# Kernel tuning notes

Measured on AMD Instinct MI355X. Metric: run time of the kernel, lower is better.

Reference implementation:

```python
import jax, jax.numpy as jnp
import numpy as np

N, E, G = 50000, 400000, 64
IN_CH, HID, H, EDGE_DIM = 128, 64, 4, 4
NEG_SLOPE = 0.2


def setup_inputs() -> dict:
    key = jax.random.key(0)
    ks = list(jax.random.split(key, 40))
    kit = iter(ks)

    def rn(shape, scale=0.05):
        return jax.random.normal(next(kit), shape, dtype=jnp.float32) * scale

    inp = {
        "x": jax.random.normal(next(kit), (N, IN_CH), dtype=jnp.float32),
        "edge_attr": jax.random.uniform(next(kit), (E, 2), dtype=jnp.float32),
        "edge_index": jax.random.randint(next(kit), (2, E), 0, N),
        "batch": jnp.sort(jax.random.randint(next(kit), (N,), 0, G)),
    }
    # edge feature fusion MLPs
    inp["W_et"] = rn((1, EDGE_DIM // 2)); inp["b_et"] = jnp.zeros((EDGE_DIM // 2,), jnp.float32)
    inp["W_uw"] = rn((1, EDGE_DIM // 2)); inp["b_uw"] = jnp.zeros((EDGE_DIM // 2,), jnp.float32)
    inp["W_ua"] = rn((1, 1));             inp["b_ua"] = jnp.zeros((1,), jnp.float32)
    # two GATv2 layers
    for li, ic in ((0, IN_CH), (1, HID)):
        inp[f"Wl{li}"] = rn((ic, H * HID)); inp[f"bl{li}"] = jnp.zeros((H * HID,), jnp.float32)
        inp[f"Wr{li}"] = rn((ic, H * HID)); inp[f"br{li}"] = jnp.zeros((H * HID,), jnp.float32)
        inp[f"att{li}"] = rn((H, HID))
        inp[f"We{li}"] = rn((EDGE_DIM, H * HID))
        inp[f"bias{li}"] = jnp.zeros((HID,), jnp.float32)
    # heads
    inp["W_fc"] = rn((HID, HID)); inp["b_fc"] = jnp.zeros((HID,), jnp.float32)
    inp["W_res"] = rn((HID, 1)); inp["b_res"] = jnp.zeros((1,), jnp.float32)
    inp["W_time"] = rn((HID, 1)); inp["b_time"] = jnp.zeros((1,), jnp.float32)
    return inp


def gatv2_layer(x, src, dst, edge_attr_proj, Wl, bl, Wr, br, att, We, bias):
    # GATv2Conv, concat=False (mean over heads)
    xl = (x @ Wl + bl).reshape(-1, H, HID)   # [N,H,C] transformed source feats
    xr = (x @ Wr + br).reshape(-1, H, HID)   # [N,H,C] transformed target feats
    ee = (edge_attr_proj @ We).reshape(-1, H, HID)  # [E,H,C]
    xj = xl[src]                              # per-edge gather of source
    m = jax.nn.leaky_relu(xj + xr[dst] + ee, NEG_SLOPE)  # [E,H,C]
    score = jnp.einsum('ehc,hc->eh', m, att)  # [E,H]
    # segment softmax over incoming edges of each destination node
    smax = jax.ops.segment_max(score, dst, num_segments=N)  # [N,H]
    ex = jnp.exp(score - smax[dst])
    denom = jax.ops.segment_sum(ex, dst, num_segments=N)
    alpha = ex / (denom[dst] + 1e-16)         # [E,H]
    out = jax.ops.segment_sum(xj * alpha[..., None], dst, num_segments=N)  # [N,H,C]
    return out.mean(axis=1) + bias            # [N,C]


def reference(x, edge_attr, W_et, b_et, W_uw, b_uw, W_ua, b_ua,
              Wl0, bl0, Wr0, br0, att0, We0, bias0,
              Wl1, bl1, Wr1, br1, att1, We1, bias1,
              W_fc, b_fc, W_res, b_res, W_time, b_time,
              edge_index, batch):
    src, dst = edge_index[0], edge_index[1]
    edge_type = edge_attr[:, 0:1]
    unwind = edge_attr[:, 1:2]
    et_emb = edge_type @ W_et + b_et
    uw_emb = unwind @ W_uw + b_uw
    uw_att = jax.nn.sigmoid(unwind @ W_ua + b_ua)
    eap = jnp.concatenate([et_emb, uw_emb * uw_att], axis=-1)  # [E,4]

    h = jax.nn.relu(gatv2_layer(x, src, dst, eap, Wl0, bl0, Wr0, br0, att0, We0, bias0))
    h = jax.nn.relu(gatv2_layer(h, src, dst, eap, Wl1, bl1, Wr1, br1, att1, We1, bias1))

    # global mean pool over graphs (dropout is identity at inference)
    sums = jax.ops.segment_sum(h, batch, num_segments=G)
    cnts = jax.ops.segment_sum(jnp.ones((h.shape[0],), h.dtype), batch, num_segments=G)
    pooled = sums / jnp.maximum(cnts, 1.0)[:, None]
    g = jax.nn.relu(pooled @ W_fc + b_fc)
    result = g @ W_res + b_res
    time = g @ W_time + b_time
    return jnp.concatenate([result, time], axis=1)  # [G,2]
```

## Files before the change

kernel.cpp:

```cpp
#include <hip/hip_runtime.h>
#include <math.h>

namespace {

constexpr int N = 50000;
constexpr int E = 400000;
constexpr int G = 64;
constexpr int HID = 64;
constexpr int HH = 256;
constexpr int NCT = 32;
constexpr float NEG = 0.2f;
constexpr int GAT_BLOCKS = 2048;
constexpr int GAT_WAVES = GAT_BLOCKS * 4;

typedef __attribute__((ext_vector_type(8))) short short8v;
typedef __attribute__((ext_vector_type(4))) float f32x4;

__device__ __forceinline__ unsigned short f2bf(float f) {
    unsigned int u = __float_as_uint(f);
    u += 0x7FFFu + ((u >> 16) & 1u);
    return (unsigned short)(u >> 16);
}
__device__ __forceinline__ float bf2f(unsigned short h) {
    return __uint_as_float(((unsigned int)h) << 16);
}
__device__ __forceinline__ float4 ld_bf4(const unsigned short* p) {
    uint2 u = *(const uint2*)p;
    float4 r;
    r.x = __uint_as_float(u.x << 16);
    r.y = __uint_as_float(u.x & 0xFFFF0000u);
    r.z = __uint_as_float(u.y << 16);
    r.w = __uint_as_float(u.y & 0xFFFF0000u);
    return r;
}

__global__ __launch_bounds__(256) void hist_k(
    const int* __restrict__ dst, int* __restrict__ deg, int* __restrict__ rank)
{
    int e = blockIdx.x * 256 + threadIdx.x;
    if (e < E) rank[e] = atomicAdd(&deg[dst[e]], 1);
}

__global__ __launch_bounds__(256) void scan1_k(
    const int* __restrict__ deg, int* __restrict__ pre, int* __restrict__ bsum)
{
    __shared__ int s[256];
    int i = blockIdx.x * 256 + threadIdx.x;
    int v = (i < N) ? deg[i] : 0;
    s[threadIdx.x] = v;
    __syncthreads();
    for (int off = 1; off < 256; off <<= 1) {
        int t = (threadIdx.x >= off) ? s[threadIdx.x - off] : 0;
        __syncthreads();
        s[threadIdx.x] += t;
        __syncthreads();
    }
    if (i < N) pre[i] = s[threadIdx.x] - v;
    if (threadIdx.x == 255) bsum[blockIdx.x] = s[255];
}

__global__ __launch_bounds__(256) void scan2_k(int* __restrict__ bsum, int nb)
{
    __shared__ int s[256];
    int tid = threadIdx.x;
    int v = (tid < nb) ? bsum[tid] : 0;
    s[tid] = v;
    __syncthreads();
    for (int off = 1; off < 256; off <<= 1) {
        int t = (tid >= off) ? s[tid - off] : 0;
        __syncthreads();
        s[tid] += t;
        __syncthreads();
    }
    if (tid < nb) bsum[tid] = s[tid] - v;
}

__global__ __launch_bounds__(256) void scatter_k(
    const int* __restrict__ src, const int* __restrict__ dst,
    const float* __restrict__ ea,
    const float* __restrict__ W_et, const float* __restrict__ b_et,
    const float* __restrict__ W_uw, const float* __restrict__ b_uw,
    const float* __restrict__ W_ua, const float* __restrict__ b_ua,
    const int* __restrict__ pre, const int* __restrict__ bsum,
    const int* __restrict__ rank,
    int* __restrict__ csr_src, float* __restrict__ eap_csr)
{
    int e = blockIdx.x * 256 + threadIdx.x;
    if (e >= E) return;
    float et = ea[e * 2 + 0], uw = ea[e * 2 + 1];
    float ua = 1.f / (1.f + expf(-(uw * W_ua[0] + b_ua[0])));
    float4 v;
    v.x = et * W_et[0] + b_et[0];
    v.y = et * W_et[1] + b_et[1];
    v.z = (uw * W_uw[0] + b_uw[0]) * ua;
    v.w = (uw * W_uw[1] + b_uw[1]) * ua;
    int d = dst[e];
    int pos = pre[d] + bsum[d >> 8] + rank[e];
    csr_src[pos] = src[e];
    *(float4*)&eap_csr[(size_t)pos * 4] = v;
}

__global__ __launch_bounds__(256) void pack_k(
    const float* __restrict__ Wl0, const float* __restrict__ Wr0,
    const float* __restrict__ bl0, const float* __restrict__ br0,
    const float* __restrict__ Wl1, const float* __restrict__ Wr1,
    const float* __restrict__ bl1, const float* __restrict__ br1,
    unsigned short* __restrict__ w0hi, unsigned short* __restrict__ w0lo,
    unsigned short* __restrict__ w1hi, unsigned short* __restrict__ w1lo,
    float* __restrict__ bc0, float* __restrict__ bc1)
{
    int idx = blockIdx.x * 256 + threadIdx.x;
    if (idx < 8192) {
        int lane = idx & 63, ct = (idx >> 6) & 31, kt = idx >> 11;
        int col = ct * 16 + (lane & 15);
        const float* W = (col < 256) ? Wl0 : Wr0;
        int c = col & 255;
        int kb = kt * 32 + ((lane >> 4) & 3) * 8;
#pragma unroll
        for (int e = 0; e < 8; e++) {
            float v = W[(size_t)(kb + e) * 256 + c];
            unsigned short hi = f2bf(v);
            unsigned short lo = f2bf(v - bf2f(hi));
            w0hi[(size_t)idx * 8 + e] = hi;
            w0lo[(size_t)idx * 8 + e] = lo;
        }
    } else if (idx < 8192 + 4096) {
        int s = idx - 8192;
        int lane = s & 63, ct = (s >> 6) & 31, kt = s >> 11;
        int col = ct * 16 + (lane & 15);
        const float* W = (col < 256) ? Wl1 : Wr1;
        int c = col & 255;
        int kb = kt * 32 + ((lane >> 4) & 3) * 8;
#pragma unroll
        for (int e = 0; e < 8; e++) {
            float v = W[(size_t)(kb + e) * 256 + c];
            unsigned short hi = f2bf(v);
            unsigned short lo = f2bf(v - bf2f(hi));
            w1hi[(size_t)s * 8 + e] = hi;
            w1lo[(size_t)s * 8 + e] = lo;
        }
    } else if (idx < 8192 + 4096 + 512) {
        int i = idx - (8192 + 4096);
        bc0[i] = (i < 256) ? bl0[i] : br0[i - 256];
    } else if (idx < 8192 + 4096 + 1024) {
        int i = idx - (8192 + 4096 + 512);
        bc1[i] = (i < 256) ? bl1[i] : br1[i - 256];
    }
}

template <int IC>
__global__ __launch_bounds__(256) void projmm_k(
    const float* __restrict__ x,
    const unsigned short* __restrict__ whi, const unsigned short* __restrict__ wlo,
    const float* __restrict__ bc,
    unsigned short* __restrict__ xlb, unsigned short* __restrict__ xrb)
{
    constexpr int KT = IC / 32;
    constexpr int LDX = IC + 4;
    constexpr int SROW = 516;
    constexpr int XS_BYTES = 32 * LDX * 4;
    constexpr int ST_BYTES = 16 * SROW * 2;
    constexpr int SMEM_BYTES = (XS_BYTES > ST_BYTES) ? XS_BYTES : ST_BYTES;
    __shared__ char smem[SMEM_BYTES];
    float (*xs)[LDX] = (float (*)[LDX])smem;
    const int base = blockIdx.x * 32;
    const int tid = threadIdx.x;
    for (int idx = tid; idx < 32 * IC / 4; idx += 256) {
        int j = idx / (IC / 4), k4 = idx - j * (IC / 4);
        int n = base + j;
        float4 v = make_float4(0.f, 0.f, 0.f, 0.f);
        if (n < N) v = *(const float4*)&x[(size_t)n * IC + k4 * 4];
        *(float4*)&xs[j][k4 * 4] = v;
    }
    __syncthreads();
    const int w = tid >> 6, lane = tid & 63;
    const int lr = lane & 15, lg = lane >> 4;
    f32x4 acc[2][8];
#pragma unroll
    for (int rt = 0; rt < 2; rt++)
#pragma unroll
        for (int ct = 0; ct < 8; ct++) {
            f32x4 z = {0.f, 0.f, 0.f, 0.f};
            acc[rt][ct] = z;
        }
#pragma unroll
    for (int kt = 0; kt < KT; kt++) {
        short8v ahi[2], alo[2];
#pragma unroll
        for (int rt = 0; rt < 2; rt++) {
            const float* p = &xs[rt * 16 + lr][kt * 32 + lg * 8];
            float4 v0 = *(const float4*)p;
            float4 v1 = *(const float4*)(p + 4);
            float fv[8] = {v0.x, v0.y, v0.z, v0.w, v1.x, v1.y, v1.z, v1.w};
            short8v h, l;
#pragma unroll
            for (int e = 0; e < 8; e++) {
                unsigned short hb = f2bf(fv[e]);
                h[e] = (short)hb;
                l[e] = (short)f2bf(fv[e] - bf2f(hb));
            }
            ahi[rt] = h;
            alo[rt] = l;
        }
        const size_t bbase = ((size_t)(kt * NCT + w * 8) * 64 + lane) * 8;
#pragma unroll
        for (int ct = 0; ct < 8; ct++) {
            short8v bhi = *(const short8v*)&whi[bbase + (size_t)ct * 64 * 8];
            short8v blo = *(const short8v*)&wlo[bbase + (size_t)ct * 64 * 8];
#pragma unroll
            for (int rt = 0; rt < 2; rt++) {
                acc[rt][ct] = __builtin_amdgcn_mfma_f32_16x16x32_bf16(ahi[rt], bhi, acc[rt][ct], 0, 0, 0);
                acc[rt][ct] = __builtin_amdgcn_mfma_f32_16x16x32_bf16(alo[rt], bhi, acc[rt][ct], 0, 0, 0);
                acc[rt][ct] = __builtin_amdgcn_mfma_f32_16x16x32_bf16(ahi[rt], blo, acc[rt][ct], 0, 0, 0);
            }
        }
    }
    __syncthreads();
    unsigned short* st = (unsigned short*)smem;
#pragma unroll
    for (int rt = 0; rt < 2; rt++) {
#pragma unroll
        for (int ct = 0; ct < 8; ct++) {
            int col = (w * 8 + ct) * 16 + lr;
            float bv = bc[col];
            f32x4 a = acc[rt][ct];
#pragma unroll
            for (int i = 0; i < 4; i++) {
                st[(lg * 4 + i) * SROW + col] = f2bf(a[i] + bv);
            }
        }
        __syncthreads();
        int rbase = base + rt * 16;
#pragma unroll
        for (int k = 0; k < 4; k++) {
            int ci = tid + k * 256;
            int rl = ci >> 6;
            int cc = (ci & 63) * 8;
            int rg = rbase + rl;
            if (rg < N) {
                uint2 lo = *(const uint2*)&st[rl * SROW + cc];
                uint2 hi = *(const uint2*)&st[rl * SROW + cc + 4];
                uint4 val = make_uint4(lo.x, lo.y, hi.x, hi.y);
                if (cc < 256) *(uint4*)&xlb[(size_t)rg * HH + cc] = val;
                else          *(uint4*)&xrb[(size_t)rg * HH + (cc - 256)] = val;
            }
        }
        __syncthreads();
    }
}

__global__ __launch_bounds__(256) void gat_aggr_k(
    const unsigned short* __restrict__ xlb, const unsigned short* __restrict__ xrb,
    const float* __restrict__ eap_csr, const float* __restrict__ We,
    const float* __restrict__ att,
    const int* __restrict__ pre, const int* __restrict__ bsum,
    const int* __restrict__ deg,
    const int* __restrict__ csr_src,
    const float* __restrict__ bias, float* __restrict__ hout)
{
    const int lane = threadIdx.x & 63;
    const int c4 = lane * 4;
    const float4 w0 = *(const float4*)&We[0 * HH + c4];
    const float4 w1 = *(const float4*)&We[1 * HH + c4];
    const float4 w2 = *(const float4*)&We[2 * HH + c4];
    const float4 w3 = *(const float4*)&We[3 * HH + c4];
    const float4 av = *(const float4*)&att[c4];
    float4 bb = make_float4(0.f, 0.f, 0.f, 0.f);
    if (lane < 16) bb = *(const float4*)&bias[c4];

    const int wid = __builtin_amdgcn_readfirstlane(blockIdx.x * 4 + (threadIdx.x >> 6));
    constexpr int q = N / GAT_WAVES;
    constexpr int r = N % GAT_WAVES;
    int d0 = wid * q + (wid < r ? wid : r);
    int dcnt = q + (wid < r ? 1 : 0);

    for (int d = d0; d < d0 + dcnt; ++d) {
        int start = pre[d] + bsum[d >> 8];
        int end = start + deg[d];
        const float4 vr = ld_bf4(&xrb[(size_t)d * HH + c4]);
        float denom = 0.f;
        float ax = 0.f, ay = 0.f, az = 0.f, aw = 0.f;
        int idx = start;
        for (; idx + 4 <= end; idx += 4) {
            int s0 = csr_src[idx], s1 = csr_src[idx + 1];
            int s2 = csr_src[idx + 2], s3 = csr_src[idx + 3];
            float4 a0 = *(const float4*)&eap_csr[(size_t)(idx + 0) * 4];
            float4 a1 = *(const float4*)&eap_csr[(size_t)(idx + 1) * 4];
            float4 a2 = *(const float4*)&eap_csr[(size_t)(idx + 2) * 4];
            float4 a3 = *(const float4*)&eap_csr[(size_t)(idx + 3) * 4];
            float4 vl0 = ld_bf4(&xlb[(size_t)s0 * HH + c4]);
            float4 vl1 = ld_bf4(&xlb[(size_t)s1 * HH + c4]);
            float4 vl2 = ld_bf4(&xlb[(size_t)s2 * HH + c4]);
            float4 vl3 = ld_bf4(&xlb[(size_t)s3 * HH + c4]);
            float p0, p1, p2, p3;
            {
                float q0 = vl0.x + vr.x + a0.x * w0.x + a0.y * w1.x + a0.z * w2.x + a0.w * w3.x;
                float q1 = vl0.y + vr.y + a0.x * w0.y + a0.y * w1.y + a0.z * w2.y + a0.w * w3.y;
                float q2 = vl0.z + vr.z + a0.x * w0.z + a0.y * w1.z + a0.z * w2.z + a0.w * w3.z;
                float q3 = vl0.w + vr.w + a0.x * w0.w + a0.y * w1.w + a0.z * w2.w + a0.w * w3.w;
                q0 = fmaxf(q0, NEG * q0); q1 = fmaxf(q1, NEG * q1);
                q2 = fmaxf(q2, NEG * q2); q3 = fmaxf(q3, NEG * q3);
                p0 = q0 * av.x + q1 * av.y + q2 * av.z + q3 * av.w;
            }
            {
                float q0 = vl1.x + vr.x + a1.x * w0.x + a1.y * w1.x + a1.z * w2.x + a1.w * w3.x;
                float q1 = vl1.y + vr.y + a1.x * w0.y + a1.y * w1.y + a1.z * w2.y + a1.w * w3.y;
                float q2 = vl1.z + vr.z + a1.x * w0.z + a1.y * w1.z + a1.z * w2.z + a1.w * w3.z;
                float q3 = vl1.w + vr.w + a1.x * w0.w + a1.y * w1.w + a1.z * w2.w + a1.w * w3.w;
                q0 = fmaxf(q0, NEG * q0); q1 = fmaxf(q1, NEG * q1);
                q2 = fmaxf(q2, NEG * q2); q3 = fmaxf(q3, NEG * q3);
                p1 = q0 * av.x + q1 * av.y + q2 * av.z + q3 * av.w;
            }
            {
                float q0 = vl2.x + vr.x + a2.x * w0.x + a2.y * w1.x + a2.z * w2.x + a2.w * w3.x;
                float q1 = vl2.y + vr.y + a2.x * w0.y + a2.y * w1.y + a2.z * w2.y + a2.w * w3.y;
                float q2 = vl2.z + vr.z + a2.x * w0.z + a2.y * w1.z + a2.z * w2.z + a2.w * w3.z;
                float q3 = vl2.w + vr.w + a2.x * w0.w + a2.y * w1.w + a2.z * w2.w + a2.w * w3.w;
                q0 = fmaxf(q0, NEG * q0); q1 = fmaxf(q1, NEG * q1);
                q2 = fmaxf(q2, NEG * q2); q3 = fmaxf(q3, NEG * q3);
                p2 = q0 * av.x + q1 * av.y + q2 * av.z + q3 * av.w;
            }
            {
                float q0 = vl3.x + vr.x + a3.x * w0.x + a3.y * w1.x + a3.z * w2.x + a3.w * w3.x;
                float q1 = vl3.y + vr.y + a3.x * w0.y + a3.y * w1.y + a3.z * w2.y + a3.w * w3.y;
                float q2 = vl3.z + vr.z + a3.x * w0.z + a3.y * w1.z + a3.z * w2.z + a3.w * w3.z;
                float q3 = vl3.w + vr.w + a3.x * w0.w + a3.y * w1.w + a3.z * w2.w + a3.w * w3.w;
                q0 = fmaxf(q0, NEG * q0); q1 = fmaxf(q1, NEG * q1);
                q2 = fmaxf(q2, NEG * q2); q3 = fmaxf(q3, NEG * q3);
                p3 = q0 * av.x + q1 * av.y + q2 * av.z + q3 * av.w;
            }
#pragma unroll
            for (int off = 1; off <= 8; off <<= 1) {
                p0 += __shfl_xor(p0, off, 64);
                p1 += __shfl_xor(p1, off, 64);
                p2 += __shfl_xor(p2, off, 64);
                p3 += __shfl_xor(p3, off, 64);
            }
            float e0 = __expf(p0);
            float e1 = __expf(p1);
            float e2 = __expf(p2);
            float e3 = __expf(p3);
            denom += e0 + e1 + e2 + e3;
            ax += e0 * vl0.x + e1 * vl1.x + e2 * vl2.x + e3 * vl3.x;
            ay += e0 * vl0.y + e1 * vl1.y + e2 * vl2.y + e3 * vl3.y;
            az += e0 * vl0.z + e1 * vl1.z + e2 * vl2.z + e3 * vl3.z;
            aw += e0 * vl0.w + e1 * vl1.w + e2 * vl2.w + e3 * vl3.w;
        }
        for (; idx < end; ++idx) {
            int s = csr_src[idx];
            float4 a = *(const float4*)&eap_csr[(size_t)idx * 4];
            float4 vl = ld_bf4(&xlb[(size_t)s * HH + c4]);
            float q0 = vl.x + vr.x + a.x * w0.x + a.y * w1.x + a.z * w2.x + a.w * w3.x;
            float q1 = vl.y + vr.y + a.x * w0.y + a.y * w1.y + a.z * w2.y + a.w * w3.y;
            float q2 = vl.z + vr.z + a.x * w0.z + a.y * w1.z + a.z * w2.z + a.w * w3.z;
            float q3 = vl.w + vr.w + a.x * w0.w + a.y * w1.w + a.z * w2.w + a.w * w3.w;
            q0 = fmaxf(q0, NEG * q0); q1 = fmaxf(q1, NEG * q1);
            q2 = fmaxf(q2, NEG * q2); q3 = fmaxf(q3, NEG * q3);
            float p = q0 * av.x + q1 * av.y + q2 * av.z + q3 * av.w;
#pragma unroll
            for (int off = 1; off <= 8; off <<= 1) p += __shfl_xor(p, off, 64);
            float e = __expf(p);
            denom += e;
            ax += e * vl.x;
            ay += e * vl.y;
            az += e * vl.z;
            aw += e * vl.w;
        }
        float inv = 0.25f / (denom + 1e-16f);
        ax *= inv; ay *= inv; az *= inv; aw *= inv;
        ax += __shfl_xor(ax, 16, 64); ax += __shfl_xor(ax, 32, 64);
        ay += __shfl_xor(ay, 16, 64); ay += __shfl_xor(ay, 32, 64);
        az += __shfl_xor(az, 16, 64); az += __shfl_xor(az, 32, 64);
        aw += __shfl_xor(aw, 16, 64); aw += __shfl_xor(aw, 32, 64);
        if (lane < 16) {
            float4 o;
            o.x = fmaxf(ax + bb.x, 0.f);
            o.y = fmaxf(ay + bb.y, 0.f);
            o.z = fmaxf(az + bb.z, 0.f);
            o.w = fmaxf(aw + bb.w, 0.f);
            *(float4*)&hout[(size_t)d * HID + c4] = o;
        }
    }
}

__global__ __launch_bounds__(256) void pool_k(
    const float* __restrict__ h, const int* __restrict__ batch,
    float* __restrict__ pooled)
{
    constexpr int CH = 16;
    int c = threadIdx.x & 63;
    int chunk = blockIdx.x * 4 + (threadIdx.x >> 6);
    int n0 = chunk * CH;
    if (n0 >= N) return;
    int nend = (n0 + CH < N) ? n0 + CH : N;
    float sum = 0.f;
    int curb = batch[n0];
    for (int n = n0; n < nend; ++n) {
        int b = batch[n];
        if (b != curb) {
            atomicAdd(&pooled[curb * HID + c], sum);
            sum = 0.f; curb = b;
        }
        sum += h[(size_t)n * HID + c];
    }
    atomicAdd(&pooled[curb * HID + c], sum);
}

__global__ __launch_bounds__(64) void head_k(
    const float* __restrict__ pooled, const int* __restrict__ batch,
    const float* __restrict__ W_fc, const float* __restrict__ b_fc,
    const float* __restrict__ W_res, const float* __restrict__ b_res,
    const float* __restrict__ W_time, const float* __restrict__ b_time,
    float* __restrict__ out)
{
    int g = blockIdx.x;
    int c = threadIdx.x;
    int lo = 0, hi = N;
    while (lo < hi) { int mid = (lo + hi) >> 1; if (batch[mid] < g) lo = mid + 1; else hi = mid; }
    int start = lo;
    hi = N;
    while (lo < hi) { int mid = (lo + hi) >> 1; if (batch[mid] < g + 1) lo = mid + 1; else hi = mid; }
    int end = lo;
    float cnt = (float)(end - start);
    float p = pooled[g * HID + c] / fmaxf(cnt, 1.0f);
    __shared__ float ps[HID];
    ps[c] = p;
    __syncthreads();
    float gv = b_fc[c];
    for (int k = 0; k < HID; k++) gv += ps[k] * W_fc[k * HID + c];
    gv = fmaxf(gv, 0.f);
    float r = gv * W_res[c];
    float t = gv * W_time[c];
#pragma unroll
    for (int off = 32; off > 0; off >>= 1) {
        r += __shfl_down(r, off, 64);
        t += __shfl_down(t, off, 64);
    }
    if (c == 0) {
        out[g * 2 + 0] = r + b_res[0];
        out[g * 2 + 1] = t + b_time[0];
    }
}

}

extern "C" void kernel_launch(void* const* d_in, const int* in_sizes, int n_in,
                              void* d_out, int out_size, void* d_ws, size_t ws_size,
                              hipStream_t stream) {
    const float* x         = (const float*)d_in[0];
    const float* edge_attr = (const float*)d_in[1];
    const int*   edge_index= (const int*)d_in[2];
    const int*   batch     = (const int*)d_in[3];
    const float* W_et = (const float*)d_in[4];
    const float* b_et = (const float*)d_in[5];
    const float* W_uw = (const float*)d_in[6];
    const float* b_uw = (const float*)d_in[7];
    const float* W_ua = (const float*)d_in[8];
    const float* b_ua = (const float*)d_in[9];
    const float* Wl0  = (const float*)d_in[10];
    const float* bl0  = (const float*)d_in[11];
    const float* Wr0  = (const float*)d_in[12];
    const float* br0  = (const float*)d_in[13];
    const float* att0 = (const float*)d_in[14];
    const float* We0  = (const float*)d_in[15];
    const float* bias0= (const float*)d_in[16];
    const float* Wl1  = (const float*)d_in[17];
    const float* bl1  = (const float*)d_in[18];
    const float* Wr1  = (const float*)d_in[19];
    const float* br1  = (const float*)d_in[20];
    const float* att1 = (const float*)d_in[21];
    const float* We1  = (const float*)d_in[22];
    const float* bias1= (const float*)d_in[23];
    const float* W_fc = (const float*)d_in[24];
    const float* b_fc = (const float*)d_in[25];
    const float* W_res= (const float*)d_in[26];
    const float* b_res= (const float*)d_in[27];
    const float* W_time=(const float*)d_in[28];
    const float* b_time=(const float*)d_in[29];

    const int* src = edge_index;
    const int* dst = edge_index + E;

    float* ws    = (float*)d_ws;
    unsigned short* xlb = (unsigned short*)ws;
    unsigned short* xrb = (unsigned short*)(ws + (size_t)N * HH);
    float* h1    = ws  + (size_t)2 * N * HH;
    float* h2    = h1  + (size_t)N * HID;
    float* pooled= h2  + (size_t)N * HID;
    int*   deg      = (int*)(pooled + (size_t)G * HID);
    int*   pre      = deg + N;
    int*   bsum     = pre + N;
    int*   rank     = bsum + 256;
    int*   csr_src  = rank + E;
    float* eap_csr  = (float*)(csr_src + E);
    unsigned short* w0hi = (unsigned short*)rank;
    unsigned short* w0lo = w0hi + 65536;
    unsigned short* w1hi = w0lo + 65536;
    unsigned short* w1lo = w1hi + 32768;
    float* bc0 = (float*)(w1lo + 32768);
    float* bc1 = bc0 + 512;

    dim3 b256(256);
    const int NB = (N + 255) / 256;
    const int NPROJ = (N + 31) / 32;

    hipMemsetAsync(pooled, 0, (size_t)(G * HID + N) * 4, stream);
    hist_k<<<(E + 255) / 256, b256, 0, stream>>>(dst, deg, rank);
    scan1_k<<<NB, b256, 0, stream>>>(deg, pre, bsum);
    scan2_k<<<1, b256, 0, stream>>>(bsum, NB);
    scatter_k<<<(E + 255) / 256, b256, 0, stream>>>(
        src, dst, edge_attr, W_et, b_et, W_uw, b_uw, W_ua, b_ua,
        pre, bsum, rank, csr_src, eap_csr);
    pack_k<<<52, b256, 0, stream>>>(Wl0, Wr0, bl0, br0, Wl1, Wr1, bl1, br1,
                                    w0hi, w0lo, w1hi, w1lo, bc0, bc1);

    projmm_k<128><<<NPROJ, b256, 0, stream>>>(x, w0hi, w0lo, bc0, xlb, xrb);
    gat_aggr_k<<<GAT_BLOCKS, b256, 0, stream>>>(
        xlb, xrb, eap_csr, We0, att0, pre, bsum, deg, csr_src, bias0, h1);

    projmm_k<64><<<NPROJ, b256, 0, stream>>>(h1, w1hi, w1lo, bc1, xlb, xrb);
    gat_aggr_k<<<GAT_BLOCKS, b256, 0, stream>>>(
        xlb, xrb, eap_csr, We1, att1, pre, bsum, deg, csr_src, bias1, h2);

    pool_k<<<((N + 15) / 16 + 3) / 4, b256, 0, stream>>>(h2, batch, pooled);
    head_k<<<G, dim3(64), 0, stream>>>(
        pooled, batch, W_fc, b_fc, W_res, b_res, W_time, b_time, (float*)d_out);
}
```

Before: 366.5 us.

## Fuse CSR construction into first-layer projection kernels to overlap and cut launches

The edge-degree histogram now runs as extra blocks of the first half of the layer-0 projection. The prefix scan runs as a single extra block of the second half. The memset is folded into the weight-pack kernel, and the two-level scan is replaced by one block that scans per-thread chunks, which removes the bsum indirection. The aim is to hide the small CSR-building kernels behind the projection GEMM and to remove several launches and serialization points. The costs are a fully serial per-thread chunk scan in one block and moving the packed weights into the unused half of the xr buffer.

```diff
diff --git a/kernel.cpp b/kernel.cpp
--- a/kernel.cpp
+++ b/kernel.cpp
@@ -13,6 +13,15 @@
 constexpr int GAT_BLOCKS = 2048;
 constexpr int GAT_WAVES = GAT_BLOCKS * 4;
 
+constexpr int NPROJ = (N + 31) / 32;
+constexpr int PH1 = 782;
+constexpr int PH1_ROWS = PH1 * 32;
+constexpr int PH2 = NPROJ - PH1;
+constexpr int HIST_BLOCKS = (E + 255) / 256;
+constexpr int PACK_BLOCKS = 52;
+constexpr int ZERO_ELEMS = G * HID + N;
+constexpr int ZERO_BLOCKS = (ZERO_ELEMS + 255) / 256;
+
 typedef __attribute__((ext_vector_type(8))) short short8v;
 typedef __attribute__((ext_vector_type(4))) float f32x4;
 
@@ -34,82 +43,23 @@
     return r;
 }
 
-__global__ __launch_bounds__(256) void hist_k(
-    const int* __restrict__ dst, int* __restrict__ deg, int* __restrict__ rank)
-{
-    int e = blockIdx.x * 256 + threadIdx.x;
-    if (e < E) rank[e] = atomicAdd(&deg[dst[e]], 1);
-}
-
-__global__ __launch_bounds__(256) void scan1_k(
-    const int* __restrict__ deg, int* __restrict__ pre, int* __restrict__ bsum)
-{
-    __shared__ int s[256];
-    int i = blockIdx.x * 256 + threadIdx.x;
-    int v = (i < N) ? deg[i] : 0;
-    s[threadIdx.x] = v;
-    __syncthreads();
-    for (int off = 1; off < 256; off <<= 1) {
-        int t = (threadIdx.x >= off) ? s[threadIdx.x - off] : 0;
-        __syncthreads();
-        s[threadIdx.x] += t;
-        __syncthreads();
-    }
-    if (i < N) pre[i] = s[threadIdx.x] - v;
-    if (threadIdx.x == 255) bsum[blockIdx.x] = s[255];
-}
-
-__global__ __launch_bounds__(256) void scan2_k(int* __restrict__ bsum, int nb)
-{
-    __shared__ int s[256];
-    int tid = threadIdx.x;
-    int v = (tid < nb) ? bsum[tid] : 0;
-    s[tid] = v;
-    __syncthreads();
-    for (int off = 1; off < 256; off <<= 1) {
-        int t = (tid >= off) ? s[tid - off] : 0;
-        __syncthreads();
-        s[tid] += t;
-        __syncthreads();
-    }
-    if (tid < nb) bsum[tid] = s[tid] - v;
-}
-
-__global__ __launch_bounds__(256) void scatter_k(
-    const int* __restrict__ src, const int* __restrict__ dst,
-    const float* __restrict__ ea,
-    const float* __restrict__ W_et, const float* __restrict__ b_et,
-    const float* __restrict__ W_uw, const float* __restrict__ b_uw,
-    const float* __restrict__ W_ua, const float* __restrict__ b_ua,
-    const int* __restrict__ pre, const int* __restrict__ bsum,
-    const int* __restrict__ rank,
-    int* __restrict__ csr_src, float* __restrict__ eap_csr)
-{
-    int e = blockIdx.x * 256 + threadIdx.x;
-    if (e >= E) return;
-    float et = ea[e * 2 + 0], uw = ea[e * 2 + 1];
-    float ua = 1.f / (1.f + expf(-(uw * W_ua[0] + b_ua[0])));
-    float4 v;
-    v.x = et * W_et[0] + b_et[0];
-    v.y = et * W_et[1] + b_et[1];
-    v.z = (uw * W_uw[0] + b_uw[0]) * ua;
-    v.w = (uw * W_uw[1] + b_uw[1]) * ua;
-    int d = dst[e];
-    int pos = pre[d] + bsum[d >> 8] + rank[e];
-    csr_src[pos] = src[e];
-    *(float4*)&eap_csr[(size_t)pos * 4] = v;
-}
-
-__global__ __launch_bounds__(256) void pack_k(
+__global__ __launch_bounds__(256) void prep_k(
     const float* __restrict__ Wl0, const float* __restrict__ Wr0,
     const float* __restrict__ bl0, const float* __restrict__ br0,
     const float* __restrict__ Wl1, const float* __restrict__ Wr1,
     const float* __restrict__ bl1, const float* __restrict__ br1,
     unsigned short* __restrict__ w0hi, unsigned short* __restrict__ w0lo,
     unsigned short* __restrict__ w1hi, unsigned short* __restrict__ w1lo,
-    float* __restrict__ bc0, float* __restrict__ bc1)
-{
-    int idx = blockIdx.x * 256 + threadIdx.x;
+    float* __restrict__ bc0, float* __restrict__ bc1,
+    int* __restrict__ zero_base)
+{
+    int b = blockIdx.x;
+    if (b >= PACK_BLOCKS) {
+        int i = (b - PACK_BLOCKS) * 256 + threadIdx.x;
+        if (i < ZERO_ELEMS) zero_base[i] = 0;
+        return;
+    }
+    int idx = b * 256 + threadIdx.x;
     if (idx < 8192) {
         int lane = idx & 63, ct = (idx >> 6) & 31, kt = idx >> 11;
         int col = ct * 16 + (lane & 15);
@@ -149,7 +99,8 @@
 }
 
 template <int IC>
-__global__ __launch_bounds__(256) void projmm_k(
+__device__ __forceinline__ void proj_body(
+    int base,
     const float* __restrict__ x,
     const unsigned short* __restrict__ whi, const unsigned short* __restrict__ wlo,
     const float* __restrict__ bc,
@@ -163,7 +114,6 @@
     constexpr int SMEM_BYTES = (XS_BYTES > ST_BYTES) ? XS_BYTES : ST_BYTES;
     __shared__ char smem[SMEM_BYTES];
     float (*xs)[LDX] = (float (*)[LDX])smem;
-    const int base = blockIdx.x * 32;
     const int tid = threadIdx.x;
     for (int idx = tid; idx < 32 * IC / 4; idx += 256) {
         int j = idx / (IC / 4), k4 = idx - j * (IC / 4);
@@ -249,12 +199,93 @@
     }
 }
 
+__global__ __launch_bounds__(256) void k1_projhist_k(
+    const float* __restrict__ x,
+    const unsigned short* __restrict__ whi, const unsigned short* __restrict__ wlo,
+    const float* __restrict__ bc,
+    unsigned short* __restrict__ xlb, unsigned short* __restrict__ xrb,
+    const int* __restrict__ dst, int* __restrict__ deg, int* __restrict__ rank)
+{
+    if (blockIdx.x < PH1) {
+        proj_body<128>(blockIdx.x * 32, x, whi, wlo, bc, xlb, xrb);
+    } else {
+        int e = (blockIdx.x - PH1) * 256 + threadIdx.x;
+        if (e < E) rank[e] = atomicAdd(&deg[dst[e]], 1);
+    }
+}
+
+__global__ __launch_bounds__(256) void k2_projscan_k(
+    const float* __restrict__ x,
+    const unsigned short* __restrict__ whi, const unsigned short* __restrict__ wlo,
+    const float* __restrict__ bc,
+    unsigned short* __restrict__ xlb, unsigned short* __restrict__ xrb,
+    const int* __restrict__ deg, int* __restrict__ pre)
+{
+    if (blockIdx.x < PH2) {
+        proj_body<128>(PH1_ROWS + blockIdx.x * 32, x, whi, wlo, bc, xlb, xrb);
+    } else {
+        constexpr int CH = 196;
+        __shared__ int sums[256];
+        int t = threadIdx.x;
+        int cbase = t * CH;
+        int cend = (cbase + CH < N) ? cbase + CH : N;
+        int s = 0;
+        for (int i = cbase; i < cend; ++i) s += deg[i];
+        sums[t] = s;
+        __syncthreads();
+        for (int off = 1; off < 256; off <<= 1) {
+            int tv = (t >= off) ? sums[t - off] : 0;
+            __syncthreads();
+            sums[t] += tv;
+            __syncthreads();
+        }
+        int run = sums[t] - s;
+        for (int i = cbase; i < cend; ++i) {
+            pre[i] = run;
+            run += deg[i];
+        }
+    }
+}
+
+__global__ __launch_bounds__(256) void scatter_k(
+    const int* __restrict__ src, const int* __restrict__ dst,
+    const float* __restrict__ ea,
+    const float* __restrict__ W_et, const float* __restrict__ b_et,
+    const float* __restrict__ W_uw, const float* __restrict__ b_uw,
+    const float* __restrict__ W_ua, const float* __restrict__ b_ua,
+    const int* __restrict__ pre, const int* __restrict__ rank,
+    int* __restrict__ csr_src, float* __restrict__ eap_csr)
+{
+    int e = blockIdx.x * 256 + threadIdx.x;
+    if (e >= E) return;
+    float et = ea[e * 2 + 0], uw = ea[e * 2 + 1];
+    float ua = 1.f / (1.f + expf(-(uw * W_ua[0] + b_ua[0])));
+    float4 v;
+    v.x = et * W_et[0] + b_et[0];
+    v.y = et * W_et[1] + b_et[1];
+    v.z = (uw * W_uw[0] + b_uw[0]) * ua;
+    v.w = (uw * W_uw[1] + b_uw[1]) * ua;
+    int d = dst[e];
+    int pos = pre[d] + rank[e];
+    csr_src[pos] = src[e];
+    *(float4*)&eap_csr[(size_t)pos * 4] = v;
+}
+
+template <int IC>
+__global__ __launch_bounds__(256) void projmm_k(
+    const float* __restrict__ x,
+    const unsigned short* __restrict__ whi, const unsigned short* __restrict__ wlo,
+    const float* __restrict__ bc,
+    unsigned short* __restrict__ xlb, unsigned short* __restrict__ xrb)
+{
+    proj_body<IC>(blockIdx.x * 32, x, whi, wlo, bc, xlb, xrb);
+}
+
 __global__ __launch_bounds__(256) void gat_aggr_k(
     const unsigned short* __restrict__ xlb, const unsigned short* __restrict__ xrb,
     const float* __restrict__ eap_csr, const float* __restrict__ We,
     const float* __restrict__ att,
-    const int* __restrict__ pre, const int* __restrict__ bsum,
-    const int* __restrict__ deg,
+    const int* __restrict__ pre, const int* __restrict__ deg,
     const int* __restrict__ csr_src,
     const float* __restrict__ bias, float* __restrict__ hout)
 {
@@ -275,7 +306,7 @@
     int dcnt = q + (wid < r ? 1 : 0);
 
     for (int d = d0; d < d0 + dcnt; ++d) {
-        int start = pre[d] + bsum[d >> 8];
+        int start = pre[d];
         int end = start + deg[d];
         const float4 vr = ld_bf4(&xrb[(size_t)d * HH + c4]);
         float denom = 0.f;
@@ -482,8 +513,15 @@
     const int* dst = edge_index + E;
 
     float* ws    = (float*)d_ws;
-    unsigned short* xlb = (unsigned short*)ws;
-    unsigned short* xrb = (unsigned short*)(ws + (size_t)N * HH);
+    unsigned short* xlb  = (unsigned short*)ws;
+    float* xr_reg = ws + (size_t)N * HH;
+    unsigned short* xrb  = (unsigned short*)xr_reg;
+    unsigned short* w0hi = (unsigned short*)xr_reg + (size_t)N * HH;
+    unsigned short* w0lo = w0hi + 65536;
+    unsigned short* w1hi = w0lo + 65536;
+    unsigned short* w1lo = w1hi + 32768;
+    float* bc0 = (float*)(w1lo + 32768);
+    float* bc1 = bc0 + 512;
     float* h1    = ws  + (size_t)2 * N * HH;
     float* h2    = h1  + (size_t)N * HID;
     float* pooled= h2  + (size_t)N * HID;
@@ -493,34 +531,29 @@
     int*   rank     = bsum + 256;
     int*   csr_src  = rank + E;
     float* eap_csr  = (float*)(csr_src + E);
-    unsigned short* w0hi = (unsigned short*)rank;
-    unsigned short* w0lo = w0hi + 65536;
-    unsigned short* w1hi = w0lo + 65536;
-    unsigned short* w1lo = w1hi + 32768;
-    float* bc0 = (float*)(w1lo + 32768);
-    float* bc1 = bc0 + 512;
 
     dim3 b256(256);
-    const int NB = (N + 255) / 256;
-    const int NPROJ = (N + 31) / 32;
-
-    hipMemsetAsync(pooled, 0, (size_t)(G * HID + N) * 4, stream);
-    hist_k<<<(E + 255) / 256, b256, 0, stream>>>(dst, deg, rank);
-    scan1_k<<<NB, b256, 0, stream>>>(deg, pre, bsum);
-    scan2_k<<<1, b256, 0, stream>>>(bsum, NB);
-    scatter_k<<<(E + 255) / 256, b256, 0, stream>>>(
+
+    prep_k<<<PACK_BLOCKS + ZERO_BLOCKS, b256, 0, stream>>>(
+        Wl0, Wr0, bl0, br0, Wl1, Wr1, bl1, br1,
+        w0hi, w0lo, w1hi, w1lo, bc0, bc1, (int*)pooled);
+
+    k1_projhist_k<<<PH1 + HIST_BLOCKS, b256, 0, stream>>>(
+        x, w0hi, w0lo, bc0, xlb, xrb, dst, deg, rank);
+
+    k2_projscan_k<<<PH2 + 1, b256, 0, stream>>>(
+        x, w0hi, w0lo, bc0, xlb, xrb, deg, pre);
+
+    scatter_k<<<HIST_BLOCKS, b256, 0, stream>>>(
         src, dst, edge_attr, W_et, b_et, W_uw, b_uw, W_ua, b_ua,
-        pre, bsum, rank, csr_src, eap_csr);
-    pack_k<<<52, b256, 0, stream>>>(Wl0, Wr0, bl0, br0, Wl1, Wr1, bl1, br1,
-                                    w0hi, w0lo, w1hi, w1lo, bc0, bc1);
-
-    projmm_k<128><<<NPROJ, b256, 0, stream>>>(x, w0hi, w0lo, bc0, xlb, xrb);
+        pre, rank, csr_src, eap_csr);
+
     gat_aggr_k<<<GAT_BLOCKS, b256, 0, stream>>>(
-        xlb, xrb, eap_csr, We0, att0, pre, bsum, deg, csr_src, bias0, h1);
+        xlb, xrb, eap_csr, We0, att0, pre, deg, csr_src, bias0, h1);
 
     projmm_k<64><<<NPROJ, b256, 0, stream>>>(h1, w1hi, w1lo, bc1, xlb, xrb);
     gat_aggr_k<<<GAT_BLOCKS, b256, 0, stream>>>(
-        xlb, xrb, eap_csr, We1, att1, pre, bsum, deg, csr_src, bias1, h2);
+        xlb, xrb, eap_csr, We1, att1, pre, deg, csr_src, bias1, h2);
 
     pool_k<<<((N + 15) / 16 + 3) / 4, b256, 0, stream>>>(h2, batch, pooled);
     head_k<<<G, dim3(64), 0, stream>>>(
```

After: 440.2 us. +20.1%, slower.
